# Performance work log

Hardware: AMD Instinct MI355X
Metric: run time of the kernel (lower is better)

Reference implementation:

```python
import jax, jax.numpy as jnp
import numpy as np

N_NODES = 100000
N_EDGES = 1600000
IN_DIM = 128
HID = 64
OUT_DIM = 16
N_GRAPHS = 500
N_STACK = 2  # layers 1..2 share shapes (HID->HID)


def _lin_init(key, fan_in, fan_out, extra=()):
    s = 1.0 / np.sqrt(fan_in)
    W = jax.random.uniform(key, extra + (fan_in, fan_out), jnp.float32, -s, s)
    b = jnp.zeros(extra + (fan_out,), jnp.float32)
    return W, b


def setup_inputs() -> dict:
    key = jax.random.key(0)
    ks = jax.random.split(key, 16)
    x = jax.random.normal(ks[0], (N_NODES, IN_DIM), jnp.float32)
    edge_index = jax.random.randint(ks[1], (2, N_EDGES), 0, N_NODES, dtype=jnp.int32)
    batch = jnp.sort(jax.random.randint(ks[2], (N_NODES,), 0, N_GRAPHS, dtype=jnp.int32))
    # layer 0: IN_DIM -> HID (query, key, value, skip)
    Wq0, bq0 = _lin_init(ks[3], IN_DIM, HID)
    Wk0, bk0 = _lin_init(ks[4], IN_DIM, HID)
    Wv0, bv0 = _lin_init(ks[5], IN_DIM, HID)
    Ws0, bs0 = _lin_init(ks[6], IN_DIM, HID)
    # layers 1..2 stacked: HID -> HID
    Wqs, bqs = _lin_init(ks[7], HID, HID, (N_STACK,))
    Wks, bks = _lin_init(ks[8], HID, HID, (N_STACK,))
    Wvs, bvs = _lin_init(ks[9], HID, HID, (N_STACK,))
    Wss, bss = _lin_init(ks[10], HID, HID, (N_STACK,))
    W1, b1 = _lin_init(ks[11], HID, HID)
    W2, b2 = _lin_init(ks[12], HID, OUT_DIM)
    return dict(x=x, Wq0=Wq0, bq0=bq0, Wk0=Wk0, bk0=bk0, Wv0=Wv0, bv0=bv0,
                Ws0=Ws0, bs0=bs0, Wqs=Wqs, bqs=bqs, Wks=Wks, bks=bks,
                Wvs=Wvs, bvs=bvs, Wss=Wss, bss=bss, W1=W1, b1=b1, W2=W2, b2=b2,
                edge_index=edge_index, batch=batch)


def _transformer_conv(x, src, dst, Wq, bq, Wk, bk, Wv, bv, Ws, bs):
    # PyG TransformerConv, heads=1, concat=True, root_weight=True, no edge_attr.
    n = x.shape[0]
    q = x @ Wq + bq  # [N, d]
    k = x @ Wk + bk
    v = x @ Wv + bv
    d = q.shape[-1]
    scores = jnp.sum(q[dst] * k[src], axis=-1) / jnp.sqrt(jnp.float32(d))  # [E]
    m = jax.ops.segment_max(scores, dst, num_segments=n)
    m = jnp.where(jnp.isfinite(m), m, 0.0)  # isolated dst nodes -> no edges anyway
    e = jnp.exp(scores - m[dst])
    denom = jax.ops.segment_sum(e, dst, num_segments=n)
    alpha = e / (denom[dst] + 1e-16)  # per-destination softmax (PyG adds 1e-16)
    agg = jax.ops.segment_sum(alpha[:, None] * v[src], dst, num_segments=n)  # [N, d]
    return agg + x @ Ws + bs


def reference(x, Wq0, bq0, Wk0, bk0, Wv0, bv0, Ws0, bs0,
              Wqs, bqs, Wks, bks, Wvs, bvs, Wss, bss,
              W1, b1, W2, b2, edge_index, batch):
    src, dst = edge_index[0], edge_index[1]
    h = jax.nn.relu(_transformer_conv(x, src, dst, Wq0, bq0, Wk0, bk0, Wv0, bv0, Ws0, bs0))
    for i in range(N_STACK):
        h = jax.nn.relu(_transformer_conv(h, src, dst, Wqs[i], bqs[i], Wks[i], bks[i],
                                          Wvs[i], bvs[i], Wss[i], bss[i]))
    pooled = jax.ops.segment_sum(h, batch, num_segments=N_GRAPHS)  # global_add_pool
    out = jax.nn.relu(pooled @ W1 + b1)
    # dropout is identity in eval mode
    return out @ W2 + b2  # [N_GRAPHS, OUT_DIM]
```

## Files before the change

kernel.cpp:

```cpp
#include <hip/hip_runtime.h>
#include <hip/hip_bf16.h>

#define N_NODES 100000
#define N_EDGES 1600000
#define IN_DIM  128
#define HID     64
#define N_GRAPHS 500

__device__ inline unsigned short f2bf(float f) {
    unsigned u = __float_as_uint(f);
    u += 0x7FFFu + ((u >> 16) & 1u);
    return (unsigned short)(u >> 16);
}
__device__ inline float bf2f(unsigned short b) {
    return __uint_as_float(((unsigned)b) << 16);
}

__device__ inline float dot64_q_bf16(float qreg, const unsigned short* __restrict__ krow) {
    const uint4* kp = (const uint4*)krow;
    uint4 kr[8];
    #pragma unroll
    for (int i = 0; i < 8; ++i) kr[i] = kp[i];
    float dot = 0.f;
    #pragma unroll
    for (int i = 0; i < 8; ++i) {
        #pragma unroll
        for (int c = 0; c < 4; ++c) {
            unsigned w = (&kr[i].x)[c];
            float qa = __shfl(qreg, i * 8 + c * 2);
            float qb = __shfl(qreg, i * 8 + c * 2 + 1);
            dot = fmaf(qa, __uint_as_float(w << 16), dot);
            dot = fmaf(qb, __uint_as_float(w & 0xFFFF0000u), dot);
        }
    }
    return dot;
}

template<int DIN>
__device__ inline void gemm_body(
    int by, int ty_blk,
    const float* __restrict__ x, int N,
    const float* __restrict__ Wq, const float* __restrict__ bq,
    const float* __restrict__ Wk, const float* __restrict__ bk,
    const float* __restrict__ Wv, const float* __restrict__ bv,
    const float* __restrict__ Ws, const float* __restrict__ bs,
    float* __restrict__ q, unsigned short* __restrict__ kb,
    unsigned short* __restrict__ vb, float* __restrict__ hout)
{
    constexpr int BM = 64, BK = 32;
    __shared__ float As[BK][BM + 1];
    __shared__ float Bs[BK][64];

    const float* W    = (by == 0) ? Wq : (by == 1) ? Wk : (by == 2) ? Wv : Ws;
    const float* bias = (by == 0) ? bq : (by == 1) ? bk : (by == 2) ? bv : bs;

    const int row0 = ty_blk * BM;
    const int tid  = threadIdx.x;
    const int tx   = (tid & 15) * 4;
    const int ty   = (tid >> 4) * 4;

    float acc[4][4] = {};

    for (int k0 = 0; k0 < DIN; k0 += BK) {
        #pragma unroll
        for (int h = 0; h < 2; ++h) {
            int idx = tid + h * 256;
            int r   = idx >> 3, c4 = idx & 7;
            int gr  = row0 + r;
            float4 val = (gr < N) ? *(const float4*)(x + (size_t)gr * DIN + k0 + c4 * 4)
                                  : make_float4(0.f, 0.f, 0.f, 0.f);
            int kk = c4 * 4;
            As[kk + 0][r] = val.x;
            As[kk + 1][r] = val.y;
            As[kk + 2][r] = val.z;
            As[kk + 3][r] = val.w;
        }
        #pragma unroll
        for (int h = 0; h < 2; ++h) {
            int kr = (tid >> 4) + h * 16;
            int n4 = (tid & 15) * 4;
            *(float4*)(&Bs[kr][n4]) = *(const float4*)(W + (size_t)(k0 + kr) * 64 + n4);
        }
        __syncthreads();

        #pragma unroll
        for (int kk = 0; kk < BK; ++kk) {
            float4 a = *(const float4*)(&As[kk][ty]);
            float4 b = *(const float4*)(&Bs[kk][tx]);
            acc[0][0] = fmaf(a.x, b.x, acc[0][0]);
            acc[0][1] = fmaf(a.x, b.y, acc[0][1]);
            acc[0][2] = fmaf(a.x, b.z, acc[0][2]);
            acc[0][3] = fmaf(a.x, b.w, acc[0][3]);
            acc[1][0] = fmaf(a.y, b.x, acc[1][0]);
            acc[1][1] = fmaf(a.y, b.y, acc[1][1]);
            acc[1][2] = fmaf(a.y, b.z, acc[1][2]);
            acc[1][3] = fmaf(a.y, b.w, acc[1][3]);
            acc[2][0] = fmaf(a.z, b.x, acc[2][0]);
            acc[2][1] = fmaf(a.z, b.y, acc[2][1]);
            acc[2][2] = fmaf(a.z, b.z, acc[2][2]);
            acc[2][3] = fmaf(a.z, b.w, acc[2][3]);
            acc[3][0] = fmaf(a.w, b.x, acc[3][0]);
            acc[3][1] = fmaf(a.w, b.y, acc[3][1]);
            acc[3][2] = fmaf(a.w, b.z, acc[3][2]);
            acc[3][3] = fmaf(a.w, b.w, acc[3][3]);
        }
        __syncthreads();
    }

    float4 bv4 = *(const float4*)(bias + tx);
    if (by == 1 || by == 2) {
        unsigned short* op = (by == 1) ? kb : vb;
        #pragma unroll
        for (int i = 0; i < 4; ++i) {
            int row = row0 + ty + i;
            if (row < N) {
                ushort4 pk;
                pk.x = f2bf(acc[i][0] + bv4.x);
                pk.y = f2bf(acc[i][1] + bv4.y);
                pk.z = f2bf(acc[i][2] + bv4.z);
                pk.w = f2bf(acc[i][3] + bv4.w);
                *(ushort4*)(op + (size_t)row * 64 + tx) = pk;
            }
        }
    } else {
        float* op = (by == 0) ? q : hout;
        #pragma unroll
        for (int i = 0; i < 4; ++i) {
            int row = row0 + ty + i;
            if (row < N) {
                float4 o = make_float4(acc[i][0] + bv4.x, acc[i][1] + bv4.y,
                                       acc[i][2] + bv4.z, acc[i][3] + bv4.w);
                *(float4*)(op + (size_t)row * 64 + tx) = o;
            }
        }
    }
}

__global__ void zero_i(int* p, int n) {
    int i = blockIdx.x * blockDim.x + threadIdx.x;
    if (i < n) p[i] = 0;
}

#define COUNT_BLOCKS 1024

__global__ __launch_bounds__(256) void gemm0_count(
    const float* __restrict__ x, int N,
    const float* __restrict__ Wq, const float* __restrict__ bq,
    const float* __restrict__ Wk, const float* __restrict__ bk,
    const float* __restrict__ Wv, const float* __restrict__ bv,
    const float* __restrict__ Ws, const float* __restrict__ bs,
    float* __restrict__ q, unsigned short* __restrict__ kb,
    unsigned short* __restrict__ vb, float* __restrict__ hout,
    const int* __restrict__ dst, int* __restrict__ counts,
    int* __restrict__ rank, int E)
{
    int bi = blockIdx.x;
    if (bi < COUNT_BLOCKS) {
        for (int e = bi * 256 + threadIdx.x; e < E; e += COUNT_BLOCKS * 256)
            rank[e] = atomicAdd(&counts[dst[e]], 1);
    } else {
        int gb = bi - COUNT_BLOCKS;
        gemm_body<IN_DIM>(gb & 3, gb >> 2, x, N, Wq, bq, Wk, bk, Wv, bv, Ws, bs,
                          q, kb, vb, hout);
    }
}

__global__ void scan1(const int* __restrict__ counts, int* __restrict__ pre,
                      int* __restrict__ blockSums, int n) {
    __shared__ int tmp[256];
    int tid = threadIdx.x;
    int i = blockIdx.x * 256 + tid;
    int v = (i < n) ? counts[i] : 0;
    tmp[tid] = v; __syncthreads();
    int acc = v;
    for (int off = 1; off < 256; off <<= 1) {
        int add = (tid >= off) ? tmp[tid - off] : 0;
        __syncthreads();
        acc += add; tmp[tid] = acc;
        __syncthreads();
    }
    if (i < n) pre[i] = acc - v;
    if (tid == 255) blockSums[blockIdx.x] = acc;
}

__global__ void scan2(int* blockSums, int nb) {
    __shared__ int tmp[512];
    int tid = threadIdx.x;
    int v = (tid < nb) ? blockSums[tid] : 0;
    tmp[tid] = v; __syncthreads();
    int acc = v;
    for (int off = 1; off < 512; off <<= 1) {
        int add = (tid >= off) ? tmp[tid - off] : 0;
        __syncthreads();
        acc += add; tmp[tid] = acc;
        __syncthreads();
    }
    if (tid < nb) blockSums[tid] = acc - v;
}

__global__ void scan3(const int* __restrict__ pre, const int* __restrict__ blockSums,
                      int* __restrict__ row_start, int n, int E) {
    int i = blockIdx.x * blockDim.x + threadIdx.x;
    if (i < n) {
        row_start[i] = pre[i] + blockSums[i >> 8];
    } else if (i == n) {
        row_start[n] = E;
    }
}

__global__ void csr_scatter(const int* __restrict__ src, const int* __restrict__ dst,
                            const int* __restrict__ rank, const int* __restrict__ row_start,
                            int* __restrict__ csr_src, int E) {
    int e = blockIdx.x * blockDim.x + threadIdx.x;
    if (e >= E) return;
    csr_src[row_start[dst[e]] + rank[e]] = src[e];
}

template<int DIN>
__global__ __launch_bounds__(256) void qkvs_gemm(
    const float* __restrict__ x, int N,
    const float* __restrict__ Wq, const float* __restrict__ bq,
    const float* __restrict__ Wk, const float* __restrict__ bk,
    const float* __restrict__ Wv, const float* __restrict__ bv,
    const float* __restrict__ Ws, const float* __restrict__ bs,
    float* __restrict__ q, unsigned short* __restrict__ kb,
    unsigned short* __restrict__ vb, float* __restrict__ hout)
{
    gemm_body<DIN>(blockIdx.x, blockIdx.y, x, N, Wq, bq, Wk, bk, Wv, bv, Ws, bs,
                   q, kb, vb, hout);
}

__global__ __launch_bounds__(256) void node_attn(
    const float* __restrict__ q, const unsigned short* __restrict__ kb,
    const unsigned short* __restrict__ vb,
    const int* __restrict__ csr_src, const int* __restrict__ row_start,
    float* __restrict__ csr_exp, float* __restrict__ hout, int N)
{
    int node = blockIdx.x * 4 + (threadIdx.x >> 6);
    int lane = threadIdx.x & 63;
    if (node >= N) return;
    int start = row_start[node], end = row_start[node + 1];
    int deg = end - start;
    size_t o = (size_t)node * 64 + lane;

    if (deg == 0) { hout[o] = fmaxf(hout[o], 0.f); return; }

    float qreg = q[o];
    float acc = 0.f;

    if (deg <= 64) {
        int s_l = (lane < deg) ? csr_src[start + lane] : 0;
        float dot = dot64_q_bf16(qreg, kb + (size_t)s_l * 64);
        float sc = (lane < deg) ? dot * 0.125f : -__builtin_inff();

        float m = sc;
        #pragma unroll
        for (int off = 1; off < 64; off <<= 1) m = fmaxf(m, __shfl_xor(m, off));

        float ex = __expf(sc - m);
        float ssum = ex;
        #pragma unroll
        for (int off = 1; off < 64; off <<= 1) ssum += __shfl_xor(ssum, off);
        float alpha = ex * (1.f / (ssum + 1e-16f));

        int j = 0;
        for (; j + 16 <= deg; j += 16) {
            float a[16]; int s[16];
            #pragma unroll
            for (int t = 0; t < 16; ++t) {
                a[t] = __shfl(alpha, j + t);
                s[t] = __shfl(s_l, j + t);
            }
            float vv[16];
            #pragma unroll
            for (int t = 0; t < 16; ++t) vv[t] = bf2f(vb[(size_t)s[t] * 64 + lane]);
            #pragma unroll
            for (int t = 0; t < 16; ++t) acc = fmaf(a[t], vv[t], acc);
        }
        for (; j + 8 <= deg; j += 8) {
            float a[8]; int s[8];
            #pragma unroll
            for (int t = 0; t < 8; ++t) {
                a[t] = __shfl(alpha, j + t);
                s[t] = __shfl(s_l, j + t);
            }
            float vv[8];
            #pragma unroll
            for (int t = 0; t < 8; ++t) vv[t] = bf2f(vb[(size_t)s[t] * 64 + lane]);
            #pragma unroll
            for (int t = 0; t < 8; ++t) acc = fmaf(a[t], vv[t], acc);
        }
        for (; j + 4 <= deg; j += 4) {
            float a[4]; int s[4];
            #pragma unroll
            for (int t = 0; t < 4; ++t) {
                a[t] = __shfl(alpha, j + t);
                s[t] = __shfl(s_l, j + t);
            }
            float vv[4];
            #pragma unroll
            for (int t = 0; t < 4; ++t) vv[t] = bf2f(vb[(size_t)s[t] * 64 + lane]);
            #pragma unroll
            for (int t = 0; t < 4; ++t) acc = fmaf(a[t], vv[t], acc);
        }
        for (; j < deg; ++j) {
            float a = __shfl(alpha, j);
            int   s = __shfl(s_l, j);
            acc = fmaf(a, bf2f(vb[(size_t)s * 64 + lane]), acc);
        }
    } else {
        float m = -__builtin_inff();
        for (int j = start + lane; j < end; j += 64) {
            int s = csr_src[j];
            float sc = dot64_q_bf16(qreg, kb + (size_t)s * 64) * 0.125f;
            csr_exp[j] = sc;
            m = fmaxf(m, sc);
        }
        #pragma unroll
        for (int off = 1; off < 64; off <<= 1) m = fmaxf(m, __shfl_xor(m, off));

        float ssum = 0.f;
        for (int j = start + lane; j < end; j += 64) {
            float ex = __expf(csr_exp[j] - m);
            csr_exp[j] = ex;
            ssum += ex;
        }
        #pragma unroll
        for (int off = 1; off < 64; off <<= 1) ssum += __shfl_xor(ssum, off);
        float inv = 1.f / (ssum + 1e-16f);

        for (int j = start; j < end; ++j) {
            int s   = csr_src[j];
            float a = csr_exp[j] * inv;
            acc = fmaf(a, bf2f(vb[(size_t)s * 64 + lane]), acc);
        }
    }

    hout[o] = fmaxf(hout[o] + acc, 0.f);
}

__global__ void zero_f(float* p, int n) {
    int i = blockIdx.x * blockDim.x + threadIdx.x;
    if (i < n) p[i] = 0.f;
}

__global__ void pool_kernel(const float* __restrict__ h, const int* __restrict__ batch,
                            float* __restrict__ pooled, int N)
{
    int col = threadIdx.x & 63;
    int rg  = threadIdx.x >> 6;
    int base = blockIdx.x * 128;
    int end  = base + 128; if (end > N) end = N;
    int gcur = -1; float acc = 0.f;
    for (int i = base + rg; i < end; i += 4) {
        int g = batch[i];
        if (g != gcur) {
            if (gcur >= 0) atomicAdd(&pooled[gcur * 64 + col], acc);
            gcur = g; acc = 0.f;
        }
        acc += h[(size_t)i * 64 + col];
    }
    if (gcur >= 0) atomicAdd(&pooled[gcur * 64 + col], acc);
}

__global__ void mlp1(const float* __restrict__ pooled, const float* __restrict__ W1,
                     const float* __restrict__ b1, float* __restrict__ hidden)
{
    int idx = blockIdx.x * blockDim.x + threadIdx.x;
    if (idx >= N_GRAPHS * 64) return;
    int g = idx >> 6, c = idx & 63;
    float acc = b1[c];
    for (int kk = 0; kk < 64; ++kk)
        acc = fmaf(pooled[g * 64 + kk], W1[kk * 64 + c], acc);
    hidden[idx] = fmaxf(acc, 0.f);
}

__global__ void mlp2(const float* __restrict__ hidden, const float* __restrict__ W2,
                     const float* __restrict__ b2, float* __restrict__ out)
{
    int idx = blockIdx.x * blockDim.x + threadIdx.x;
    if (idx >= N_GRAPHS * 16) return;
    int g = idx >> 4, c = idx & 15;
    float acc = b2[c];
    for (int kk = 0; kk < 64; ++kk)
        acc = fmaf(hidden[g * 64 + kk], W2[kk * 16 + c], acc);
    out[idx] = acc;
}

extern "C" void kernel_launch(void* const* d_in, const int* in_sizes, int n_in,
                              void* d_out, int out_size, void* d_ws, size_t ws_size,
                              hipStream_t stream)
{
    const float* x   = (const float*)d_in[0];
    const float* Wq0 = (const float*)d_in[1];  const float* bq0 = (const float*)d_in[2];
    const float* Wk0 = (const float*)d_in[3];  const float* bk0 = (const float*)d_in[4];
    const float* Wv0 = (const float*)d_in[5];  const float* bv0 = (const float*)d_in[6];
    const float* Ws0 = (const float*)d_in[7];  const float* bs0 = (const float*)d_in[8];
    const float* Wqs = (const float*)d_in[9];  const float* bqs = (const float*)d_in[10];
    const float* Wks = (const float*)d_in[11]; const float* bks = (const float*)d_in[12];
    const float* Wvs = (const float*)d_in[13]; const float* bvs = (const float*)d_in[14];
    const float* Wss = (const float*)d_in[15]; const float* bss = (const float*)d_in[16];
    const float* W1  = (const float*)d_in[17]; const float* b1  = (const float*)d_in[18];
    const float* W2  = (const float*)d_in[19]; const float* b2  = (const float*)d_in[20];
    const int*   ei  = (const int*)d_in[21];
    const int*   batch = (const int*)d_in[22];
    float* out = (float*)d_out;

    const int* src = ei;
    const int* dst = ei + N_EDGES;

    const size_t NH = (size_t)N_NODES * 64;
    float* q        = (float*)d_ws;
    float* hA       = q + NH;
    float* hB       = hA + NH;
    float* csr_exp  = hB + NH;
    int*   csr_src  = (int*)(csr_exp + N_EDGES);
    int*   rank     = csr_src + N_EDGES;
    unsigned short* kb = (unsigned short*)(rank + N_EDGES);
    unsigned short* vb = kb + NH;
    int*   row_start= (int*)(vb + NH);
    int*   counts   = row_start + N_NODES + 1;
    int*   blockSums= counts + N_NODES;
    float* pooled   = (float*)(blockSums + 512);
    float* hidden   = pooled + N_GRAPHS * 64;

    struct LW { const float *Wq,*bq,*Wk,*bk,*Wv,*bv,*Ws,*bs; };
    LW lw[3] = {
        { Wq0, bq0, Wk0, bk0, Wv0, bv0, Ws0, bs0 },
        { Wqs, bqs, Wks, bks, Wvs, bvs, Wss, bss },
        { Wqs + 4096, bqs + 64, Wks + 4096, bks + 64, Wvs + 4096, bvs + 64, Wss + 4096, bss + 64 }
    };

    const int nodeBlocks = (N_NODES + 255) / 256;
    const int edgeBlocks = (N_EDGES + 255) / 256;
    const int scanBlocks = (N_NODES + 255) / 256;
    const int rowTiles   = (N_NODES + 63) / 64;
    const int gemmBlocks = 4 * rowTiles;

    zero_i<<<nodeBlocks, 256, 0, stream>>>(counts, N_NODES);
    gemm0_count<<<COUNT_BLOCKS + gemmBlocks, 256, 0, stream>>>(
        x, N_NODES,
        lw[0].Wq, lw[0].bq, lw[0].Wk, lw[0].bk, lw[0].Wv, lw[0].bv, lw[0].Ws, lw[0].bs,
        q, kb, vb, hA,
        dst, counts, rank, N_EDGES);

    scan1<<<scanBlocks, 256, 0, stream>>>(counts, counts, blockSums, N_NODES);
    scan2<<<1, 512, 0, stream>>>(blockSums, scanBlocks);
    scan3<<<(N_NODES + 256) / 256, 256, 0, stream>>>(counts, blockSums, row_start,
                                                     N_NODES, N_EDGES);
    csr_scatter<<<edgeBlocks, 256, 0, stream>>>(src, dst, rank, row_start, csr_src, N_EDGES);

    node_attn<<<(N_NODES + 3) / 4, 256, 0, stream>>>(q, kb, vb, csr_src, row_start,
                                                     csr_exp, hA, N_NODES);

    const dim3 gemmGrid(4, rowTiles);
    for (int L = 1; L < 3; ++L) {
        const float* hin = (L == 1) ? hA : hB;
        float* hou       = (L == 1) ? hB : hA;
        qkvs_gemm<HID><<<gemmGrid, 256, 0, stream>>>(hin, N_NODES,
            lw[L].Wq, lw[L].bq, lw[L].Wk, lw[L].bk, lw[L].Wv, lw[L].bv, lw[L].Ws, lw[L].bs,
            q, kb, vb, hou);
        node_attn<<<(N_NODES + 3) / 4, 256, 0, stream>>>(q, kb, vb, csr_src, row_start,
                                                         csr_exp, hou, N_NODES);
    }

    zero_f<<<(N_GRAPHS * 64 + 255) / 256, 256, 0, stream>>>(pooled, N_GRAPHS * 64);
    pool_kernel<<<(N_NODES + 127) / 128, 256, 0, stream>>>(hA, batch, pooled, N_NODES);
    mlp1<<<(N_GRAPHS * 64 + 255) / 256, 256, 0, stream>>>(pooled, W1, b1, hidden);
    mlp2<<<(N_GRAPHS * 16 + 255) / 256, 256, 0, stream>>>(hidden, W2, b2, out);
}
```

Before: 669.1 us.

## Process each node with a 32-lane half-wave handling two features per lane

The node attention kernel now assigns 32 lanes per destination node instead of a full 64-lane wavefront. Each lane owns two feature columns and loads them as one 32-bit bf16 pair from V and as a float2 from q and hout. Eight nodes run per block. The intent is to double node parallelism per wave and halve the per-edge gather instruction count for the low average degree of about 16. The trade-off is that the register fast path now covers degree up to 32 instead of 64, so more nodes fall into the slower global-memory softmax path. The 64-wide shuffles are replaced with width-32 shuffles.

```diff
diff --git a/kernel.cpp b/kernel.cpp
--- a/kernel.cpp
+++ b/kernel.cpp
@@ -16,7 +16,7 @@
     return __uint_as_float(((unsigned)b) << 16);
 }
 
-__device__ inline float dot64_q_bf16(float qreg, const unsigned short* __restrict__ krow) {
+__device__ inline float dot64_q2_bf16(float2 qreg, const unsigned short* __restrict__ krow) {
     const uint4* kp = (const uint4*)krow;
     uint4 kr[8];
     #pragma unroll
@@ -27,8 +27,8 @@
         #pragma unroll
         for (int c = 0; c < 4; ++c) {
             unsigned w = (&kr[i].x)[c];
-            float qa = __shfl(qreg, i * 8 + c * 2);
-            float qb = __shfl(qreg, i * 8 + c * 2 + 1);
+            float qa = __shfl(qreg.x, 4 * i + c, 32);
+            float qb = __shfl(qreg.y, 4 * i + c, 32);
             dot = fmaf(qa, __uint_as_float(w << 16), dot);
             dot = fmaf(qb, __uint_as_float(w & 0xFFFF0000u), dot);
         }
@@ -236,31 +236,36 @@
     const int* __restrict__ csr_src, const int* __restrict__ row_start,
     float* __restrict__ csr_exp, float* __restrict__ hout, int N)
 {
-    int node = blockIdx.x * 4 + (threadIdx.x >> 6);
-    int lane = threadIdx.x & 63;
+    int node = blockIdx.x * 8 + (threadIdx.x >> 5);
+    int lane = threadIdx.x & 31;
     if (node >= N) return;
     int start = row_start[node], end = row_start[node + 1];
     int deg = end - start;
-    size_t o = (size_t)node * 64 + lane;
-
-    if (deg == 0) { hout[o] = fmaxf(hout[o], 0.f); return; }
-
-    float qreg = q[o];
-    float acc = 0.f;
-
-    if (deg <= 64) {
+    size_t ob = (size_t)node * 64 + 2 * lane;
+
+    float2 hv = *(const float2*)(hout + ob);
+    if (deg == 0) {
+        hv.x = fmaxf(hv.x, 0.f); hv.y = fmaxf(hv.y, 0.f);
+        *(float2*)(hout + ob) = hv;
+        return;
+    }
+
+    float2 qreg = *(const float2*)(q + ob);
+    float2 acc = make_float2(0.f, 0.f);
+
+    if (deg <= 32) {
         int s_l = (lane < deg) ? csr_src[start + lane] : 0;
-        float dot = dot64_q_bf16(qreg, kb + (size_t)s_l * 64);
+        float dot = dot64_q2_bf16(qreg, kb + (size_t)s_l * 64);
         float sc = (lane < deg) ? dot * 0.125f : -__builtin_inff();
 
         float m = sc;
         #pragma unroll
-        for (int off = 1; off < 64; off <<= 1) m = fmaxf(m, __shfl_xor(m, off));
+        for (int off = 1; off < 32; off <<= 1) m = fmaxf(m, __shfl_xor(m, off, 32));
 
         float ex = __expf(sc - m);
         float ssum = ex;
         #pragma unroll
-        for (int off = 1; off < 64; off <<= 1) ssum += __shfl_xor(ssum, off);
+        for (int off = 1; off < 32; off <<= 1) ssum += __shfl_xor(ssum, off, 32);
         float alpha = ex * (1.f / (ssum + 1e-16f));
 
         int j = 0;
@@ -268,75 +273,93 @@
             float a[16]; int s[16];
             #pragma unroll
             for (int t = 0; t < 16; ++t) {
-                a[t] = __shfl(alpha, j + t);
-                s[t] = __shfl(s_l, j + t);
-            }
-            float vv[16];
-            #pragma unroll
-            for (int t = 0; t < 16; ++t) vv[t] = bf2f(vb[(size_t)s[t] * 64 + lane]);
-            #pragma unroll
-            for (int t = 0; t < 16; ++t) acc = fmaf(a[t], vv[t], acc);
+                a[t] = __shfl(alpha, j + t, 32);
+                s[t] = __shfl(s_l, j + t, 32);
+            }
+            unsigned w[16];
+            #pragma unroll
+            for (int t = 0; t < 16; ++t)
+                w[t] = *(const unsigned*)(vb + (size_t)s[t] * 64 + 2 * lane);
+            #pragma unroll
+            for (int t = 0; t < 16; ++t) {
+                acc.x = fmaf(a[t], __uint_as_float(w[t] << 16), acc.x);
+                acc.y = fmaf(a[t], __uint_as_float(w[t] & 0xFFFF0000u), acc.y);
+            }
         }
         for (; j + 8 <= deg; j += 8) {
             float a[8]; int s[8];
             #pragma unroll
             for (int t = 0; t < 8; ++t) {
-                a[t] = __shfl(alpha, j + t);
-                s[t] = __shfl(s_l, j + t);
-            }
-            float vv[8];
-            #pragma unroll
-            for (int t = 0; t < 8; ++t) vv[t] = bf2f(vb[(size_t)s[t] * 64 + lane]);
-            #pragma unroll
-            for (int t = 0; t < 8; ++t) acc = fmaf(a[t], vv[t], acc);
+                a[t] = __shfl(alpha, j + t, 32);
+                s[t] = __shfl(s_l, j + t, 32);
+            }
+            unsigned w[8];
+            #pragma unroll
+            for (int t = 0; t < 8; ++t)
+                w[t] = *(const unsigned*)(vb + (size_t)s[t] * 64 + 2 * lane);
+            #pragma unroll
+            for (int t = 0; t < 8; ++t) {
+                acc.x = fmaf(a[t], __uint_as_float(w[t] << 16), acc.x);
+                acc.y = fmaf(a[t], __uint_as_float(w[t] & 0xFFFF0000u), acc.y);
+            }
         }
         for (; j + 4 <= deg; j += 4) {
             float a[4]; int s[4];
             #pragma unroll
             for (int t = 0; t < 4; ++t) {
-                a[t] = __shfl(alpha, j + t);
-                s[t] = __shfl(s_l, j + t);
-            }
-            float vv[4];
-            #pragma unroll
-            for (int t = 0; t < 4; ++t) vv[t] = bf2f(vb[(size_t)s[t] * 64 + lane]);
-            #pragma unroll
-            for (int t = 0; t < 4; ++t) acc = fmaf(a[t], vv[t], acc);
+                a[t] = __shfl(alpha, j + t, 32);
+                s[t] = __shfl(s_l, j + t, 32);
+            }
+            unsigned w[4];
+            #pragma unroll
+            for (int t = 0; t < 4; ++t)
+                w[t] = *(const unsigned*)(vb + (size_t)s[t] * 64 + 2 * lane);
+            #pragma unroll
+            for (int t = 0; t < 4; ++t) {
+                acc.x = fmaf(a[t], __uint_as_float(w[t] << 16), acc.x);
+                acc.y = fmaf(a[t], __uint_as_float(w[t] & 0xFFFF0000u), acc.y);
+            }
         }
         for (; j < deg; ++j) {
-            float a = __shfl(alpha, j);
-            int   s = __shfl(s_l, j);
-            acc = fmaf(a, bf2f(vb[(size_t)s * 64 + lane]), acc);
+            float a = __shfl(alpha, j, 32);
+            int   s = __shfl(s_l, j, 32);
+            unsigned w = *(const unsigned*)(vb + (size_t)s * 64 + 2 * lane);
+            acc.x = fmaf(a, __uint_as_float(w << 16), acc.x);
+            acc.y = fmaf(a, __uint_as_float(w & 0xFFFF0000u), acc.y);
         }
     } else {
         float m = -__builtin_inff();
-        for (int j = start + lane; j < end; j += 64) {
+        for (int j = start + lane; j < end; j += 32) {
             int s = csr_src[j];
-            float sc = dot64_q_bf16(qreg, kb + (size_t)s * 64) * 0.125f;
+            float sc = dot64_q2_bf16(qreg, kb + (size_t)s * 64) * 0.125f;
             csr_exp[j] = sc;
             m = fmaxf(m, sc);
         }
         #pragma unroll
-        for (int off = 1; off < 64; off <<= 1) m = fmaxf(m, __shfl_xor(m, off));
+        for (int off = 1; off < 32; off <<= 1) m = fmaxf(m, __shfl_xor(m, off, 32));
 
         float ssum = 0.f;
-        for (int j = start + lane; j < end; j += 64) {
+        for (int j = start + lane; j < end; j += 32) {
             float ex = __expf(csr_exp[j] - m);
             csr_exp[j] = ex;
             ssum += ex;
         }
         #pragma unroll
-        for (int off = 1; off < 64; off <<= 1) ssum += __shfl_xor(ssum, off);
+        for (int off = 1; off < 32; off <<= 1) ssum += __shfl_xor(ssum, off, 32);
         float inv = 1.f / (ssum + 1e-16f);
 
         for (int j = start; j < end; ++j) {
             int s   = csr_src[j];
             float a = csr_exp[j] * inv;
-            acc = fmaf(a, bf2f(vb[(size_t)s * 64 + lane]), acc);
-        }
-    }
-
-    hout[o] = fmaxf(hout[o] + acc, 0.f);
+            unsigned w = *(const unsigned*)(vb + (size_t)s * 64 + 2 * lane);
+            acc.x = fmaf(a, __uint_as_float(w << 16), acc.x);
+            acc.y = fmaf(a, __uint_as_float(w & 0xFFFF0000u), acc.y);
+        }
+    }
+
+    hv.x = fmaxf(hv.x + acc.x, 0.f);
+    hv.y = fmaxf(hv.y + acc.y, 0.f);
+    *(float2*)(hout + ob) = hv;
 }
 
 __global__ void zero_f(float* p, int n) {
@@ -450,7 +473,7 @@
                                                      N_NODES, N_EDGES);
     csr_scatter<<<edgeBlocks, 256, 0, stream>>>(src, dst, rank, row_start, csr_src, N_EDGES);
 
-    node_attn<<<(N_NODES + 3) / 4, 256, 0, stream>>>(q, kb, vb, csr_src, row_start,
+    node_attn<<<(N_NODES + 7) / 8, 256, 0, stream>>>(q, kb, vb, csr_src, row_start,
                                                      csr_exp, hA, N_NODES);
 
     const dim3 gemmGrid(4, rowTiles);
@@ -460,7 +483,7 @@
         qkvs_gemm<HID><<<gemmGrid, 256, 0, stream>>>(hin, N_NODES,
             lw[L].Wq, lw[L].bq, lw[L].Wk, lw[L].bk, lw[L].Wv, lw[L].bv, lw[L].Ws, lw[L].bs,
             q, kb, vb, hou);
-        node_attn<<<(N_NODES + 3) / 4, 256, 0, stream>>>(q, kb, vb, csr_src, row_start,
+        node_attn<<<(N_NODES + 7) / 8, 256, 0, stream>>>(q, kb, vb, csr_src, row_start,
                                                          csr_exp, hou, N_NODES);
     }
 
```

Result: faster. 577.2 us (median of 2 runs) (-13.7%).
